# Performance work log

Measured on AMD Instinct MI355X. Metric: run time of the kernel, lower is better.

Reference implementation:

```python
import jax, jax.numpy as jnp
import numpy as np

COLOR_SIZE = 4
SIZE = 128
LENGTH = SIZE * SIZE * 3  # 49152


def setup_inputs() -> dict:
    key = jax.random.key(0)
    k1, k2, k3, k4 = jax.random.split(key, 4)
    example = jax.random.randint(k1, (2, SIZE, SIZE, 3), 0, COLOR_SIZE, dtype=jnp.int32)
    W_in = jax.random.normal(k2, (1, 1024), dtype=jnp.float32) * 0.02
    pos_enc = jax.random.normal(k3, (LENGTH, 1024), dtype=jnp.float32)
    W_final = jax.random.normal(k4, (1024, COLOR_SIZE), dtype=jnp.float32) * 0.02
    b_final = jnp.zeros((COLOR_SIZE,), dtype=jnp.float32)
    return {"example": example, "W_in": W_in, "pos_enc": pos_enc,
            "W_final": W_final, "b_final": b_final}


def reference(example, W_in, pos_enc, W_final, b_final):
    # example: [B, 128, 128, 3] int, values in [0, color_size)
    B = example.shape[0]
    x = example.astype(jnp.float32) / COLOR_SIZE * 2.0 - 1.0
    x = x.reshape(B, LENGTH, 1)
    x = x * 2.0 - 1.0  # second scaling, as in original call()
    x = x @ W_in  # [B, L, 1] @ [1, F] -> [B, L, F]
    x = jax.nn.relu(x + pos_enc)
    # running-average via causal cumsum; factor computed in fp16 as in original
    factor = (1.0 / jnp.arange(1, LENGTH + 1, dtype=jnp.float32))
    factor = factor.astype(jnp.float16).astype(jnp.float32)[:, None]
    x = jnp.cumsum(x, axis=-2) * factor
    x = x @ W_final + b_final  # [B, L, color_size]
    x = x.reshape(B, SIZE, SIZE, 3, COLOR_SIZE)
    return x.astype(jnp.float32)
```

## Files before the change

kernel.cpp:

```cpp
#include <hip/hip_runtime.h>
#include <hip/hip_fp16.h>
#include <math.h>

#define L_TOTAL 49152
#define TILE 512
#define NTILES 96

__device__ __forceinline__ float4 f4add(float4 a, float4 b) {
  return make_float4(a.x + b.x, a.y + b.y, a.z + b.z, a.w + b.w);
}

__device__ __forceinline__ float fp16_roundtrip_pos(float x) {
  unsigned u = __float_as_uint(x);
  int e = (int)((u >> 23) & 0xffu) - 127;
  unsigned m = (u & 0x7fffffu) | 0x800000u;
  int shift = (e >= -14) ? 13 : (13 + (-14 - e));
  if (shift >= 25) return 0.0f;
  unsigned keep = m >> shift;
  unsigned rem = m & ((1u << shift) - 1u);
  unsigned halfbit = 1u << (shift - 1);
  if (rem > halfbit || (rem == halfbit && (keep & 1u))) keep++;
  return ldexpf((float)keep, e + shift - 23);
}

__global__ __launch_bounds__(256, 4) void compute_g_kernel(
    const int* __restrict__ ex, const float4* __restrict__ win4,
    const float4* __restrict__ pos4, const float4* __restrict__ wf4,
    float4* __restrict__ g4) {
  const int lane = threadIdx.x & 63;
  const int wave = threadIdx.x >> 6;
  const int rowBase = blockIdx.x * 64 + wave * 16;

  float4 win[4];
  float4 wf[4][4];
#pragma unroll
  for (int j = 0; j < 4; ++j) {
    const int fi = j * 64 + lane;
    win[j] = win4[fi];
#pragma unroll
    for (int k = 0; k < 4; ++k) wf[j][k] = wf4[fi * 4 + k];
  }

  for (int r = 0; r < 16; ++r) {
    const int l = rowBase + r;
    const float s0 = (float)ex[l] - 3.0f;
    const float s1 = (float)ex[L_TOTAL + l] - 3.0f;
    float4 a0 = make_float4(0.f, 0.f, 0.f, 0.f);
    float4 a1 = make_float4(0.f, 0.f, 0.f, 0.f);
#pragma unroll
    for (int j = 0; j < 4; ++j) {
      const float4 p = pos4[(size_t)l * 256 + j * 64 + lane];
      const float pc[4] = {p.x, p.y, p.z, p.w};
      const float wc[4] = {win[j].x, win[j].y, win[j].z, win[j].w};
#pragma unroll
      for (int k = 0; k < 4; ++k) {
        const float t0 = fmaxf(fmaf(s0, wc[k], pc[k]), 0.0f);
        const float t1 = fmaxf(fmaf(s1, wc[k], pc[k]), 0.0f);
        const float4 w = wf[j][k];
        a0.x = fmaf(t0, w.x, a0.x); a0.y = fmaf(t0, w.y, a0.y);
        a0.z = fmaf(t0, w.z, a0.z); a0.w = fmaf(t0, w.w, a0.w);
        a1.x = fmaf(t1, w.x, a1.x); a1.y = fmaf(t1, w.y, a1.y);
        a1.z = fmaf(t1, w.z, a1.z); a1.w = fmaf(t1, w.w, a1.w);
      }
    }
#pragma unroll
    for (int off = 32; off > 0; off >>= 1) {
      a0.x += __shfl_xor(a0.x, off); a0.y += __shfl_xor(a0.y, off);
      a0.z += __shfl_xor(a0.z, off); a0.w += __shfl_xor(a0.w, off);
      a1.x += __shfl_xor(a1.x, off); a1.y += __shfl_xor(a1.y, off);
      a1.z += __shfl_xor(a1.z, off); a1.w += __shfl_xor(a1.w, off);
    }
    if (lane == 0) {
      g4[l] = a0;
      g4[L_TOTAL + l] = a1;
    }
  }
}

__global__ __launch_bounds__(256) void tile_sums_kernel(
    const float4* __restrict__ g4, float4* __restrict__ tsum) {
  const int t = blockIdx.x;
  const int b = blockIdx.y;
  const int tid = threadIdx.x;
  const float4* base = g4 + (size_t)b * L_TOTAL + (size_t)t * TILE;
  float4 v = f4add(base[tid], base[tid + 256]);
#pragma unroll
  for (int off = 32; off > 0; off >>= 1) {
    v.x += __shfl_xor(v.x, off); v.y += __shfl_xor(v.y, off);
    v.z += __shfl_xor(v.z, off); v.w += __shfl_xor(v.w, off);
  }
  __shared__ float4 ws[4];
  if ((tid & 63) == 0) ws[tid >> 6] = v;
  __syncthreads();
  if (tid == 0) {
    tsum[b * NTILES + t] = f4add(f4add(ws[0], ws[1]), f4add(ws[2], ws[3]));
  }
}

__global__ __launch_bounds__(256) void scan_tiles_kernel(
    const float4* __restrict__ tsum, float4* __restrict__ toff) {
  __shared__ float4 buf[2][128];
  const int b = threadIdx.x >> 7;
  const int i = threadIdx.x & 127;
  float4 v = make_float4(0.f, 0.f, 0.f, 0.f);
  if (i < NTILES) v = tsum[b * NTILES + i];
  buf[b][i] = v;
  __syncthreads();
#pragma unroll
  for (int d = 1; d < 128; d <<= 1) {
    float4 t = make_float4(0.f, 0.f, 0.f, 0.f);
    if (i >= d) t = buf[b][i - d];
    __syncthreads();
    if (i >= d) buf[b][i] = f4add(buf[b][i], t);
    __syncthreads();
  }
  if (i < NTILES)
    toff[b * NTILES + i] = (i == 0) ? make_float4(0.f, 0.f, 0.f, 0.f)
                                    : buf[b][i - 1];
}

__global__ __launch_bounds__(512) void scan_out_kernel(
    const float4* __restrict__ g4, const float4* __restrict__ toff,
    const float* __restrict__ b_final, float4* __restrict__ out4) {
  const int t = blockIdx.x;
  const int b = blockIdx.y;
  const int tid = threadIdx.x;
  const int lane = tid & 63;
  const int wv = tid >> 6;
  const int l = t * TILE + tid;
  float4 v = g4[(size_t)b * L_TOTAL + l];
#pragma unroll
  for (int d = 1; d < 64; d <<= 1) {
    const float ux = __shfl_up(v.x, d);
    const float uy = __shfl_up(v.y, d);
    const float uz = __shfl_up(v.z, d);
    const float uw = __shfl_up(v.w, d);
    if (lane >= d) { v.x += ux; v.y += uy; v.z += uz; v.w += uw; }
  }
  __shared__ float4 wsum[8];
  __shared__ float4 woff[8];
  if (lane == 63) wsum[wv] = v;
  __syncthreads();
  if (tid == 0) {
    float4 run = make_float4(0.f, 0.f, 0.f, 0.f);
#pragma unroll
    for (int w = 0; w < 8; ++w) { woff[w] = run; run = f4add(run, wsum[w]); }
  }
  __syncthreads();
  const float4 base = f4add(woff[wv], toff[b * NTILES + t]);
  v = f4add(v, base);
  const float factor = fp16_roundtrip_pos(1.0f / (float)(l + 1));
  const float4 bf = make_float4(b_final[0], b_final[1], b_final[2], b_final[3]);
  float4 o;
  o.x = fmaf(v.x, factor, bf.x);
  o.y = fmaf(v.y, factor, bf.y);
  o.z = fmaf(v.z, factor, bf.z);
  o.w = fmaf(v.w, factor, bf.w);
  out4[(size_t)b * L_TOTAL + l] = o;
}

extern "C" void kernel_launch(void* const* d_in, const int* in_sizes, int n_in,
                              void* d_out, int out_size, void* d_ws, size_t ws_size,
                              hipStream_t stream) {
  const int* ex = (const int*)d_in[0];
  const float4* win4 = (const float4*)d_in[1];
  const float4* pos4 = (const float4*)d_in[2];
  const float4* wf4 = (const float4*)d_in[3];
  const float* bfin = (const float*)d_in[4];

  float4* g4 = (float4*)d_ws;
  float4* tsum = (float4*)((char*)d_ws + (size_t)2 * L_TOTAL * sizeof(float4));
  float4* toff = tsum + 2 * NTILES;

  compute_g_kernel<<<L_TOTAL / 64, 256, 0, stream>>>(ex, win4, pos4, wf4, g4);
  tile_sums_kernel<<<dim3(NTILES, 2), 256, 0, stream>>>(g4, tsum);
  scan_tiles_kernel<<<1, 256, 0, stream>>>(tsum, toff);
  scan_out_kernel<<<dim3(NTILES, 2), 512, 0, stream>>>(g4, toff, bfin,
                                                       (float4*)d_out);
}
```

Baseline: 50.97 us.

## Fuse tile sums into compute kernel and merge scan into two launches

The compute kernel now covers 96 rows per block across 512 blocks, stages each row's result in shared memory, and also writes a per-block partial sum. This removes the separate tile-sum and tile-scan kernels. The final kernel works out each block's prefix offset by summing the earlier block partials directly, then runs a shared-memory scan over its 96 rows. This cuts kernel launches from four to two, but each later block re-reads up to 512 partials, and the Hillis-Steele scan syncs at every step.

Result: faster. 48.01 us (-5.8%).

```diff
diff --git a/kernel.cpp b/kernel.cpp
--- a/kernel.cpp
+++ b/kernel.cpp
@@ -1,10 +1,10 @@
 #include <hip/hip_runtime.h>
-#include <hip/hip_fp16.h>
 #include <math.h>
 
 #define L_TOTAL 49152
-#define TILE 512
-#define NTILES 96
+#define NBLK 512
+#define ROWS_PER_BLK 96
+#define ROWS_PER_WAVE 24
 
 __device__ __forceinline__ float4 f4add(float4 a, float4 b) {
   return make_float4(a.x + b.x, a.y + b.y, a.z + b.z, a.w + b.w);
@@ -23,13 +23,16 @@
   return ldexpf((float)keep, e + shift - 23);
 }
 
-__global__ __launch_bounds__(256, 4) void compute_g_kernel(
+__global__ __launch_bounds__(256, 2) void gpart_kernel(
     const int* __restrict__ ex, const float4* __restrict__ win4,
     const float4* __restrict__ pos4, const float4* __restrict__ wf4,
-    float4* __restrict__ g4) {
+    float4* __restrict__ g4, float4* __restrict__ pp) {
+  __shared__ float4 sg[2][ROWS_PER_BLK];
+  __shared__ float4 wpart[2][4];
+
   const int lane = threadIdx.x & 63;
-  const int wave = threadIdx.x >> 6;
-  const int rowBase = blockIdx.x * 64 + wave * 16;
+  const int wv = threadIdx.x >> 6;
+  const int rowBase = blockIdx.x * ROWS_PER_BLK + wv * ROWS_PER_WAVE;
 
   float4 win[4];
   float4 wf[4][4];
@@ -41,7 +44,10 @@
     for (int k = 0; k < 4; ++k) wf[j][k] = wf4[fi * 4 + k];
   }
 
-  for (int r = 0; r < 16; ++r) {
+  float4 bp0 = make_float4(0.f, 0.f, 0.f, 0.f);
+  float4 bp1 = make_float4(0.f, 0.f, 0.f, 0.f);
+
+  for (int r = 0; r < ROWS_PER_WAVE; ++r) {
     const int l = rowBase + r;
     const float s0 = (float)ex[l] - 3.0f;
     const float s1 = (float)ex[L_TOTAL + l] - 3.0f;
@@ -70,93 +76,91 @@
       a1.x += __shfl_xor(a1.x, off); a1.y += __shfl_xor(a1.y, off);
       a1.z += __shfl_xor(a1.z, off); a1.w += __shfl_xor(a1.w, off);
     }
+    bp0 = f4add(bp0, a0);
+    bp1 = f4add(bp1, a1);
     if (lane == 0) {
-      g4[l] = a0;
-      g4[L_TOTAL + l] = a1;
+      sg[0][wv * ROWS_PER_WAVE + r] = a0;
+      sg[1][wv * ROWS_PER_WAVE + r] = a1;
     }
+  }
+
+  if (lane == 0) { wpart[0][wv] = bp0; wpart[1][wv] = bp1; }
+  __syncthreads();
+
+  if (threadIdx.x < 2 * ROWS_PER_BLK) {
+    const int bb = threadIdx.x / ROWS_PER_BLK;
+    const int i = threadIdx.x - bb * ROWS_PER_BLK;
+    g4[(size_t)bb * L_TOTAL + blockIdx.x * ROWS_PER_BLK + i] = sg[bb][i];
+  }
+  if (threadIdx.x < 2) {
+    const int bb = threadIdx.x;
+    pp[bb * NBLK + blockIdx.x] =
+        f4add(f4add(wpart[bb][0], wpart[bb][1]),
+              f4add(wpart[bb][2], wpart[bb][3]));
   }
 }
 
-__global__ __launch_bounds__(256) void tile_sums_kernel(
-    const float4* __restrict__ g4, float4* __restrict__ tsum) {
-  const int t = blockIdx.x;
-  const int b = blockIdx.y;
-  const int tid = threadIdx.x;
-  const float4* base = g4 + (size_t)b * L_TOTAL + (size_t)t * TILE;
-  float4 v = f4add(base[tid], base[tid + 256]);
-#pragma unroll
-  for (int off = 32; off > 0; off >>= 1) {
-    v.x += __shfl_xor(v.x, off); v.y += __shfl_xor(v.y, off);
-    v.z += __shfl_xor(v.z, off); v.w += __shfl_xor(v.w, off);
-  }
-  __shared__ float4 ws[4];
-  if ((tid & 63) == 0) ws[tid >> 6] = v;
-  __syncthreads();
-  if (tid == 0) {
-    tsum[b * NTILES + t] = f4add(f4add(ws[0], ws[1]), f4add(ws[2], ws[3]));
-  }
-}
+__global__ __launch_bounds__(256, 2) void scan_kernel(
+    const float4* __restrict__ g4, const float4* __restrict__ pp,
+    const float* __restrict__ bfin, float4* __restrict__ out4) {
+  __shared__ float4 sg[2][ROWS_PER_BLK];
+  __shared__ float4 wq[2][4];
+  __shared__ float4 boffs[2];
 
-__global__ __launch_bounds__(256) void scan_tiles_kernel(
-    const float4* __restrict__ tsum, float4* __restrict__ toff) {
-  __shared__ float4 buf[2][128];
-  const int b = threadIdx.x >> 7;
-  const int i = threadIdx.x & 127;
-  float4 v = make_float4(0.f, 0.f, 0.f, 0.f);
-  if (i < NTILES) v = tsum[b * NTILES + i];
-  buf[b][i] = v;
-  __syncthreads();
-#pragma unroll
-  for (int d = 1; d < 128; d <<= 1) {
-    float4 t = make_float4(0.f, 0.f, 0.f, 0.f);
-    if (i >= d) t = buf[b][i - d];
-    __syncthreads();
-    if (i >= d) buf[b][i] = f4add(buf[b][i], t);
-    __syncthreads();
-  }
-  if (i < NTILES)
-    toff[b * NTILES + i] = (i == 0) ? make_float4(0.f, 0.f, 0.f, 0.f)
-                                    : buf[b][i - 1];
-}
-
-__global__ __launch_bounds__(512) void scan_out_kernel(
-    const float4* __restrict__ g4, const float4* __restrict__ toff,
-    const float* __restrict__ b_final, float4* __restrict__ out4) {
-  const int t = blockIdx.x;
-  const int b = blockIdx.y;
   const int tid = threadIdx.x;
   const int lane = tid & 63;
   const int wv = tid >> 6;
-  const int l = t * TILE + tid;
-  float4 v = g4[(size_t)b * L_TOTAL + l];
+  const int bid = blockIdx.x;
+
+  if (tid < 2 * ROWS_PER_BLK) {
+    const int bb = tid / ROWS_PER_BLK;
+    const int i = tid - bb * ROWS_PER_BLK;
+    sg[bb][i] = g4[(size_t)bb * L_TOTAL + bid * ROWS_PER_BLK + i];
+  }
+
+  float4 q0 = make_float4(0.f, 0.f, 0.f, 0.f);
+  float4 q1 = make_float4(0.f, 0.f, 0.f, 0.f);
+  for (int jj = tid; jj < bid; jj += 256) {
+    q0 = f4add(q0, pp[jj]);
+    q1 = f4add(q1, pp[NBLK + jj]);
+  }
 #pragma unroll
-  for (int d = 1; d < 64; d <<= 1) {
-    const float ux = __shfl_up(v.x, d);
-    const float uy = __shfl_up(v.y, d);
-    const float uz = __shfl_up(v.z, d);
-    const float uw = __shfl_up(v.w, d);
-    if (lane >= d) { v.x += ux; v.y += uy; v.z += uz; v.w += uw; }
+  for (int off = 32; off > 0; off >>= 1) {
+    q0.x += __shfl_xor(q0.x, off); q0.y += __shfl_xor(q0.y, off);
+    q0.z += __shfl_xor(q0.z, off); q0.w += __shfl_xor(q0.w, off);
+    q1.x += __shfl_xor(q1.x, off); q1.y += __shfl_xor(q1.y, off);
+    q1.z += __shfl_xor(q1.z, off); q1.w += __shfl_xor(q1.w, off);
   }
-  __shared__ float4 wsum[8];
-  __shared__ float4 woff[8];
-  if (lane == 63) wsum[wv] = v;
+  if (lane == 0) { wq[0][wv] = q0; wq[1][wv] = q1; }
   __syncthreads();
   if (tid == 0) {
-    float4 run = make_float4(0.f, 0.f, 0.f, 0.f);
-#pragma unroll
-    for (int w = 0; w < 8; ++w) { woff[w] = run; run = f4add(run, wsum[w]); }
+    boffs[0] = f4add(f4add(wq[0][0], wq[0][1]), f4add(wq[0][2], wq[0][3]));
+    boffs[1] = f4add(f4add(wq[1][0], wq[1][1]), f4add(wq[1][2], wq[1][3]));
   }
   __syncthreads();
-  const float4 base = f4add(woff[wv], toff[b * NTILES + t]);
-  v = f4add(v, base);
-  const float factor = fp16_roundtrip_pos(1.0f / (float)(l + 1));
-  const float4 bf = make_float4(b_final[0], b_final[1], b_final[2], b_final[3]);
-  float4 o;
-  o.x = fmaf(v.x, factor, bf.x);
-  o.y = fmaf(v.y, factor, bf.y);
-  o.z = fmaf(v.z, factor, bf.z);
-  o.w = fmaf(v.w, factor, bf.w);
-  out4[(size_t)b * L_TOTAL + l] = o;
+
+  const bool act = tid < 2 * ROWS_PER_BLK;
+  const int bb = tid / ROWS_PER_BLK;
+  const int i = tid - bb * ROWS_PER_BLK;
+#pragma unroll
+  for (int d = 1; d < ROWS_PER_BLK; d <<= 1) {
+    float4 addv = make_float4(0.f, 0.f, 0.f, 0.f);
+    if (act && i >= d) addv = sg[bb][i - d];
+    __syncthreads();
+    if (act && i >= d) sg[bb][i] = f4add(sg[bb][i], addv);
+    __syncthreads();
+  }
+  if (act) {
+    const int l = bid * ROWS_PER_BLK + i;
+    const float4 v = f4add(sg[bb][i], boffs[bb]);
+    const float factor = fp16_roundtrip_pos(1.0f / (float)(l + 1));
+    float4 o;
+    o.x = fmaf(v.x, factor, bfin[0]);
+    o.y = fmaf(v.y, factor, bfin[1]);
+    o.z = fmaf(v.z, factor, bfin[2]);
+    o.w = fmaf(v.w, factor, bfin[3]);
+    out4[(size_t)bb * L_TOTAL + l] = o;
+  }
 }
 
 extern "C" void kernel_launch(void* const* d_in, const int* in_sizes, int n_in,
@@ -167,14 +171,11 @@
   const float4* pos4 = (const float4*)d_in[2];
   const float4* wf4 = (const float4*)d_in[3];
   const float* bfin = (const float*)d_in[4];
+  float4* out4 = (float4*)d_out;
 
   float4* g4 = (float4*)d_ws;
-  float4* tsum = (float4*)((char*)d_ws + (size_t)2 * L_TOTAL * sizeof(float4));
-  float4* toff = tsum + 2 * NTILES;
+  float4* pp = g4 + (size_t)2 * L_TOTAL;
 
-  compute_g_kernel<<<L_TOTAL / 64, 256, 0, stream>>>(ex, win4, pos4, wf4, g4);
-  tile_sums_kernel<<<dim3(NTILES, 2), 256, 0, stream>>>(g4, tsum);
-  scan_tiles_kernel<<<1, 256, 0, stream>>>(tsum, toff);
-  scan_out_kernel<<<dim3(NTILES, 2), 512, 0, stream>>>(g4, toff, bfin,
-                                                       (float4*)d_out);
+  gpart_kernel<<<NBLK, 256, 0, stream>>>(ex, win4, pos4, wf4, g4, pp);
+  scan_kernel<<<NBLK, 256, 0, stream>>>(g4, pp, bfin, out4);
 }
```
